# Optimization experiments

Measured on AMD Instinct MI355X. Metric: run time of the kernel, lower is better.

Reference implementation:

```python
import jax, jax.numpy as jnp
from jax import lax
import numpy as np

B, N, DIM = 2, 2048, 1024
HEADS, DIM_HEAD = 16, 64
KERNELS = (0, 3, 5, 7)
GROUPS = len(KERNELS)
HPG = HEADS // GROUPS          # heads per group = 4
CG = HPG * DIM_HEAD            # channels per group for depthwise conv = 256
INNER = HEADS * DIM_HEAD       # 1024


def _alibi_slopes(n):
    # power-of-2 branch of LearnedAlibiPosBias._get_slopes (n=4 here)
    start = 2.0 ** (-(2.0 ** -(np.log2(n) - 3)))
    return np.array([start * start ** i for i in range(n)], dtype=np.float32)


def setup_inputs() -> dict:
    key = jax.random.key(0)
    ks = jax.random.split(key, 24)
    d = {}
    d['x'] = jax.random.normal(ks[0], (B, N, DIM), jnp.float32)
    d['ln_gamma'] = jnp.ones((DIM,), jnp.float32)
    d['ln_beta'] = jnp.zeros((DIM,), jnp.float32)
    d['w_qkv'] = jax.random.normal(ks[1], (3 * INNER, DIM), jnp.float32) * 0.02
    i = 2
    for p in ('q', 'k', 'v'):
        for ksz in (3, 5, 7):
            d[f'dw{p}_w{ksz}'] = jax.random.normal(ks[i], (CG, 1, ksz), jnp.float32) * 0.1; i += 1
            d[f'dw{p}_b{ksz}'] = jax.random.normal(ks[i], (CG,), jnp.float32) * 0.02; i += 1
    # learned alibi slopes, initialized to the standard ALiBi values per group
    sl = _alibi_slopes(HPG).reshape(1, HPG, 1, 1)
    d['slopes'] = jnp.asarray(np.tile(sl, (GROUPS, 1, 1, 1)))
    d['w_out'] = jax.random.normal(ks[20], (DIM, INNER), jnp.float32) * 0.02
    return d


def _dw_causal_conv(xg, w, b, ksz):
    # xg: (B, CG, N); depthwise causal conv, left pad ksz-1
    xg = jnp.pad(xg, ((0, 0), (0, 0), (ksz - 1, 0)))
    out = lax.conv_general_dilated(xg, w, (1,), 'VALID',
                                   feature_group_count=CG,
                                   dimension_numbers=('NCH', 'OIH', 'NCH'))
    return out + b[None, :, None]


def _grouped_conv(t, w3, b3, w5, b5, w7, b7):
    # t: (B, INNER, N) channels laid out head-major; group g = channels [g*CG,(g+1)*CG)
    parts = [t[:, :CG]]  # group 0: kernel_size 0 -> Identity
    for i, (w, b, ksz) in enumerate(((w3, b3, 3), (w5, b5, 5), (w7, b7, 7))):
        parts.append(_dw_causal_conv(t[:, (i + 1) * CG:(i + 2) * CG], w, b, ksz))
    out = jnp.concatenate(parts, axis=1)                      # (B, INNER, N)
    out = out.reshape(B, HEADS, DIM_HEAD, N)
    return jnp.transpose(out, (0, 1, 3, 2))                   # (B, H, N, Dh)


def _forward(x, ln_gamma, ln_beta, w_qkv,
             dwq_w3, dwq_b3, dwq_w5, dwq_b5, dwq_w7, dwq_b7,
             dwk_w3, dwk_b3, dwk_w5, dwk_b5, dwk_w7, dwk_b7,
             dwv_w3, dwv_b3, dwv_w5, dwv_b5, dwv_w7, dwv_b7,
             slopes, w_out):
    scale = DIM_HEAD ** -0.5
    mu = jnp.mean(x, axis=-1, keepdims=True)
    var = jnp.var(x, axis=-1, keepdims=True)
    h = (x - mu) * lax.rsqrt(var + 1e-5) * ln_gamma + ln_beta   # (B, N, DIM)
    qkv = jnp.einsum('bnd,ed->ben', h, w_qkv)                   # (B, 3*INNER, N)
    q, k, v = jnp.split(qkv, 3, axis=1)
    q = _grouped_conv(q, dwq_w3, dwq_b3, dwq_w5, dwq_b5, dwq_w7, dwq_b7)
    k = _grouped_conv(k, dwk_w3, dwk_b3, dwk_w5, dwk_b5, dwk_w7, dwk_b7)
    v = _grouped_conv(v, dwv_w3, dwv_b3, dwv_w5, dwv_b5, dwv_w7, dwv_b7)
    sim = jnp.einsum('bhid,bhjd->bhij', q * scale, k)           # (B, H, N, N)
    idx = jnp.arange(N)
    dist = -jnp.abs(idx[None, :] - idx[:, None]).astype(sim.dtype)  # (N, N)
    bias = slopes.reshape(HEADS, 1, 1) * dist[None]             # (H, N, N)
    sim = sim + bias[None]
    causal = idx[None, :] > idx[:, None]                        # strictly future
    sim = jnp.where(causal[None, None], -jnp.finfo(sim.dtype).max, sim)
    attn = jax.nn.softmax(sim, axis=-1)
    out = jnp.einsum('bhij,bhjd->bhid', attn, v)                # (B, H, N, Dh)
    out = jnp.transpose(out, (0, 2, 1, 3)).reshape(B, N, INNER)
    return jnp.einsum('bne,de->bnd', out, w_out)


def reference(x, ln_gamma, ln_beta, w_qkv,
              dwq_w3, dwq_b3, dwq_w5, dwq_b5, dwq_w7, dwq_b7,
              dwk_w3, dwk_b3, dwk_w5, dwk_b5, dwk_w7, dwk_b7,
              dwv_w3, dwv_b3, dwv_w5, dwv_b5, dwv_w7, dwv_b7,
              slopes, w_out):
    return _forward(x, ln_gamma, ln_beta, w_qkv,
                    dwq_w3, dwq_b3, dwq_w5, dwq_b5, dwq_w7, dwq_b7,
                    dwk_w3, dwk_b3, dwk_w5, dwk_b5, dwk_w7, dwk_b7,
                    dwv_w3, dwv_b3, dwv_w5, dwv_b5, dwv_w7, dwv_b7,
                    slopes, w_out)
```

## Files before the change

### kernel.cpp

```cpp
#include <hip/hip_runtime.h>
#include <hip/hip_bf16.h>
#include <stdint.h>

typedef __bf16 bf8 __attribute__((ext_vector_type(8)));
typedef float  f4  __attribute__((ext_vector_type(4)));

constexpr int BATCH  = 2;
constexpr int SEQ    = 2048;
constexpr int DMODEL = 1024;
constexpr int NH     = 16;
constexpr int DHEAD  = 64;
constexpr int E3     = 3072;

static __device__ __forceinline__ f4 mfma16(bf8 a, bf8 b, f4 c){
  return __builtin_amdgcn_mfma_f32_16x16x32_bf16(a, b, c, 0, 0, 0);
}
static __device__ __forceinline__ uint32_t pack2(float a, float b){
  union { __bf16 h[2]; uint32_t u; } p;
  p.h[0] = (__bf16)a; p.h[1] = (__bf16)b;
  return p.u;
}
typedef const __attribute__((address_space(1))) uint32_t g_u32;
typedef __attribute__((address_space(3))) uint32_t l_u32;
static __device__ __forceinline__ void glds16(const __bf16* g, __bf16* l){
  __builtin_amdgcn_global_load_lds((g_u32*)g, (l_u32*)l, 16, 0, 0);
}

__global__ __launch_bounds__(256) void prep_kernel(const float* __restrict__ x,
                                                   const float* __restrict__ gam,
                                                   const float* __restrict__ bet,
                                                   __bf16* __restrict__ h,
                                                   const float* __restrict__ wq,
                                                   __bf16* __restrict__ wqb){
  int bid = blockIdx.x;
  int tid = threadIdx.x;
  if(bid >= BATCH*SEQ){
    int i = ((bid - BATCH*SEQ) * 256 + tid) * 4;
    float4 v = *(const float4*)(wq + i);
    __bf16 o[4] = {(__bf16)v.x, (__bf16)v.y, (__bf16)v.z, (__bf16)v.w};
    *(uint2*)(wqb + i) = *(const uint2*)o;
    return;
  }
  int row = bid;
  const float* xr = x + (size_t)row * DMODEL;
  float4 v = *(const float4*)(xr + tid*4);
  float s = v.x + v.y + v.z + v.w;
  float ss = v.x*v.x + v.y*v.y + v.z*v.z + v.w*v.w;
#pragma unroll
  for(int m=1;m<64;m<<=1){ s += __shfl_xor(s, m); ss += __shfl_xor(ss, m); }
  __shared__ float sm[8];
  int wid = tid >> 6;
  if((tid & 63) == 0){ sm[wid] = s; sm[4+wid] = ss; }
  __syncthreads();
  s  = sm[0]+sm[1]+sm[2]+sm[3];
  ss = sm[4]+sm[5]+sm[6]+sm[7];
  float mu  = s * (1.f/DMODEL);
  float var = ss * (1.f/DMODEL) - mu*mu;
  float r = rsqrtf(var + 1e-5f);
  float4 g = *(const float4*)(gam + tid*4);
  float4 bb = *(const float4*)(bet + tid*4);
  __bf16 o[4] = { (__bf16)((v.x-mu)*r*g.x + bb.x), (__bf16)((v.y-mu)*r*g.y + bb.y),
                  (__bf16)((v.z-mu)*r*g.z + bb.z), (__bf16)((v.w-mu)*r*g.w + bb.w) };
  *(uint2*)(h + (size_t)row*DMODEL + tid*4) = *(uint2*)o;
}

template<typename CT>
__global__ __launch_bounds__(256) void gemm_nt(const __bf16* __restrict__ A,
                                               const __bf16* __restrict__ Bm,
                                               CT* __restrict__ C,
                                               int M, int Ncols, int K){
  __shared__ __align__(16) __bf16 smem[4*128*32];
  __bf16* As0 = smem;
  __bf16* Bs0 = smem + 2*128*32;
  int nwgx = gridDim.x;
  int nwg  = nwgx * gridDim.y;
  int bidl = blockIdx.y * nwgx + blockIdx.x;
  int swz  = (bidl & 7) * (nwg >> 3) + (bidl >> 3);
  int m0 = (swz / nwgx) * 128, n0 = (swz % nwgx) * 128;
  int tid = threadIdx.x;
  int lane = tid & 63, wid = tid >> 6;
  int quad = lane >> 4, l15 = lane & 15;
  int wm = (wid >> 1) * 64, wn = (wid & 1) * 64;
  f4 acc[4][4] = {};
  int r0 = wid*32 + (lane >> 2);
  int cofs = (lane & 3) * 8;
  const __bf16* ag = A  + (size_t)(m0 + r0) * K + cofs;
  const __bf16* bg = Bm + (size_t)(n0 + r0) * K + cofs;
  const int d0 = (wid*32)*32, d1 = (wid*32+16)*32;
  const size_t rowskip = (size_t)16 * K;
  glds16(ag,           As0 + d0);
  glds16(ag + rowskip, As0 + d1);
  glds16(bg,           Bs0 + d0);
  glds16(bg + rowskip, Bs0 + d1);
  __syncthreads();
  int cur = 0;
  for(int k0 = 0; k0 < K; k0 += 32){
    int k1 = k0 + 32;
    if(k1 < K){
      int nb = cur ^ 1;
      glds16(ag + k1,           As0 + nb*128*32 + d0);
      glds16(ag + rowskip + k1, As0 + nb*128*32 + d1);
      glds16(bg + k1,           Bs0 + nb*128*32 + d0);
      glds16(bg + rowskip + k1, Bs0 + nb*128*32 + d1);
    }
    const __bf16* AsC = As0 + cur*128*32;
    const __bf16* BsC = Bs0 + cur*128*32;
    bf8 af[4], bfr[4];
#pragma unroll
    for(int i=0;i<4;i++){
      af[i]  = *(const bf8*)&AsC[(wm + i*16 + l15)*32 + quad*8];
      bfr[i] = *(const bf8*)&BsC[(wn + i*16 + l15)*32 + quad*8];
    }
#pragma unroll
    for(int mi=0;mi<4;mi++)
#pragma unroll
      for(int ni=0;ni<4;ni++)
        acc[mi][ni] = mfma16(af[mi], bfr[ni], acc[mi][ni]);
    __syncthreads();
    cur ^= 1;
  }
  if constexpr (sizeof(CT) == 2){
    __bf16* scr = smem;
    uint32_t* sp = (uint32_t*)smem;
#pragma unroll
    for(int qq=0; qq<4; qq++){
      __syncthreads();
      if((wid>>1) == (qq>>1)){
        int mi0 = (qq & 1) * 2;
#pragma unroll
        for(int mm=0; mm<2; mm++){
          int mi = mi0 + mm;
#pragma unroll
          for(int ni=0; ni<4; ni++)
#pragma unroll
            for(int r=0; r<4; r++){
              int lr = (mi - mi0)*16 + quad*4 + r;
              scr[lr*136 + wn + ni*16 + l15] = (__bf16)acc[mi][ni][r];
            }
        }
      }
      __syncthreads();
#pragma unroll
      for(int it=0; it<2; it++){
        int idx = it*256 + tid;
        int row = idx >> 4;
        int ck  = idx & 15;
        uint4 v = { sp[row*68 + ck*4 + 0], sp[row*68 + ck*4 + 1],
                    sp[row*68 + ck*4 + 2], sp[row*68 + ck*4 + 3] };
        *(uint4*)(C + (size_t)(m0 + qq*32 + row)*Ncols + n0 + ck*8) = v;
      }
    }
  } else {
    float* scr = (float*)smem;
#pragma unroll
    for(int qq=0; qq<4; qq++){
      __syncthreads();
      if((wid>>1) == (qq>>1)){
        int mi0 = (qq & 1) * 2;
#pragma unroll
        for(int mm=0; mm<2; mm++){
          int mi = mi0 + mm;
#pragma unroll
          for(int ni=0; ni<4; ni++)
#pragma unroll
            for(int r=0; r<4; r++){
              int lr = (mi - mi0)*16 + quad*4 + r;
              scr[lr*136 + wn + ni*16 + l15] = acc[mi][ni][r];
            }
        }
      }
      __syncthreads();
#pragma unroll
      for(int it=0; it<4; it++){
        int idx = it*256 + tid;
        int row = idx >> 5;
        int ck  = idx & 31;
        float4 v = { scr[row*136 + ck*4 + 0], scr[row*136 + ck*4 + 1],
                     scr[row*136 + ck*4 + 2], scr[row*136 + ck*4 + 3] };
        *(float4*)(C + (size_t)(m0 + qq*32 + row)*Ncols + n0 + ck*4) = v;
      }
    }
  }
}

__global__ __launch_bounds__(256) void conv_kernel(const __bf16* __restrict__ qkv,
    __bf16* __restrict__ qo, __bf16* __restrict__ ko, __bf16* __restrict__ vt,
    const float* qw3,const float* qb3,const float* qw5,const float* qb5,const float* qw7,const float* qb7,
    const float* kw3,const float* kb3,const float* kw5,const float* kb5,const float* kw7,const float* kb7,
    const float* vw3,const float* vb3,const float* vw5,const float* vb5,const float* vw7,const float* vb7){
  __shared__ __align__(16) __bf16 tile[72*256];
  int nc = blockIdx.x;
  int ec = blockIdx.y;
  int b  = blockIdx.z;
  int tid = threadIdx.x;
  int n0 = nc * 64;
  {
    int rrow = tid >> 5;
    int ccol = (tid & 31) * 8;
    const __bf16* src = qkv + (size_t)b*SEQ*E3 + ec*256 + ccol;
#pragma unroll
    for(int p=0;p<9;p++){
      int row = p*8 + rrow;
      int n = n0 - 8 + row;
      uint4 v = {0u,0u,0u,0u};
      if(n >= 0) v = *(const uint4*)(src + (size_t)n*E3);
      *(uint4*)&tile[row*256 + ccol] = v;
    }
  }
  __syncthreads();
  int p = ec >> 2;
  int g = ec & 3;
  float w0=0.f,w1=0.f,w2=0.f,w3=0.f,w4=0.f,w5=0.f,w6=0.f,bias=0.f;
  if(g == 1){
    const float* wp = (p==0)? qw3 : (p==1)? kw3 : vw3;
    const float* bp = (p==0)? qb3 : (p==1)? kb3 : vb3;
    w0 = wp[tid*3+0]; w1 = wp[tid*3+1]; w2 = wp[tid*3+2]; bias = bp[tid];
  } else if(g == 2){
    const float* wp = (p==0)? qw5 : (p==1)? kw5 : vw5;
    const float* bp = (p==0)? qb5 : (p==1)? kb5 : vb5;
    w0 = wp[tid*5+0]; w1 = wp[tid*5+1]; w2 = wp[tid*5+2];
    w3 = wp[tid*5+3]; w4 = wp[tid*5+4]; bias = bp[tid];
  } else if(g == 3){
    const float* wp = (p==0)? qw7 : (p==1)? kw7 : vw7;
    const float* bp = (p==0)? qb7 : (p==1)? kb7 : vb7;
    w0 = wp[tid*7+0]; w1 = wp[tid*7+1]; w2 = wp[tid*7+2]; w3 = wp[tid*7+3];
    w4 = wp[tid*7+4]; w5 = wp[tid*7+5]; w6 = wp[tid*7+6]; bias = bp[tid];
  }
  float x0 = (float)tile[2*256 + tid];
  float x1 = (float)tile[3*256 + tid];
  float x2 = (float)tile[4*256 + tid];
  float x3 = (float)tile[5*256 + tid];
  float x4 = (float)tile[6*256 + tid];
  float x5 = (float)tile[7*256 + tid];
#define CONV_STEP(cur, o)                                                      \
  { if(g == 0)      o = (cur);                                                 \
    else if(g == 1) o = w0*x4 + w1*x5 + w2*(cur) + bias;                       \
    else if(g == 2) o = w0*x2 + w1*x3 + w2*x4 + w3*x5 + w4*(cur) + bias;       \
    else            o = w0*x0 + w1*x1 + w2*x2 + w3*x3 + w4*x4 + w5*x5          \
                        + w6*(cur) + bias;                                     \
    x0=x1; x1=x2; x2=x3; x3=x4; x4=x5; x5=(cur); }
  uint32_t vout[32];
#pragma unroll
  for(int blk=0; blk<8; blk++){
#pragma unroll
    for(int up=0; up<4; up++){
      float ca = (float)tile[(8 + blk*8 + up*2    )*256 + tid];
      float oa; CONV_STEP(ca, oa);
      float cb = (float)tile[(8 + blk*8 + up*2 + 1)*256 + tid];
      float ob; CONV_STEP(cb, ob);
      vout[blk*4 + up] = pack2(oa, ob);
    }
  }
#undef CONV_STEP
  __syncthreads();
  uint32_t* ot = (uint32_t*)tile;
#pragma unroll
  for(int j=0;j<32;j++) ot[tid*33 + j] = vout[j];
  __syncthreads();
  if(p == 2){
#pragma unroll
    for(int it=0; it<8; it++){
      int idx = it*256 + tid;
      int ch  = idx >> 3;
      int ncq = idx & 7;
      uint4 val = { ot[ch*33 + ncq*4 + 0], ot[ch*33 + ncq*4 + 1],
                    ot[ch*33 + ncq*4 + 2], ot[ch*33 + ncq*4 + 3] };
      int hh2 = g*4 + (ch >> 6);
      int dh2 = ch & 63;
      *(uint4*)(vt + ((size_t)((b*NH + hh2)*DHEAD + dh2))*SEQ + n0 + ncq*8) = val;
    }
  } else {
    __bf16* outp = (p==0) ? qo : ko;
#pragma unroll
    for(int it=0; it<8; it++){
      int idx = it*256 + tid;
      int lh  = idx >> 9;
      int dn  = (idx >> 3) & 63;
      int ck  = idx & 7;
      int j   = dn >> 1;
      int sh  = (dn & 1) * 16;
      uint32_t hv[8];
#pragma unroll
      for(int m=0;m<8;m++)
        hv[m] = (ot[(lh*64 + ck*8 + m)*33 + j] >> sh) & 0xffffu;
      uint4 val = { hv[0] | (hv[1]<<16), hv[2] | (hv[3]<<16),
                    hv[4] | (hv[5]<<16), hv[6] | (hv[7]<<16) };
      int hh2 = g*4 + lh;
      *(uint4*)(outp + ((size_t)(b*NH + hh2)*SEQ + n0 + dn)*DHEAD + ck*8) = val;
    }
  }
}

__global__ __launch_bounds__(256, 3) void attn_kernel(const __bf16* __restrict__ Qin,
                                                      const __bf16* __restrict__ Kin,
                                                      const __bf16* __restrict__ Vtin,
                                                      const float* __restrict__ slopes,
                                                      __bf16* __restrict__ Oout,
                                                      const float* __restrict__ wsrc,
                                                      __bf16* __restrict__ wdst){
  __shared__ __align__(16) __bf16 Ks[2][64*64];
  __shared__ __align__(16) __bf16 Vts[2][64*64];
  __shared__ __align__(16) __bf16 Ps[4][16*72];
  __shared__ float Al[4][16];
  int bid = blockIdx.x;
  int tid = threadIdx.x;
  if(bid >= 1024){
    int i = ((bid - 1024) * 256 + tid) * 4;
    float4 v = *(const float4*)(wsrc + i);
    __bf16 o[4] = {(__bf16)v.x, (__bf16)v.y, (__bf16)v.z, (__bf16)v.w};
    *(uint2*)(wdst + i) = *(const uint2*)o;
    return;
  }
  int qi = 31 - (bid >> 5);
  int by = (bid & 7) + ((bid >> 3) & 3) * 8;
  int b  = by >> 4, hh = by & 15;
  int lane = tid & 63, w = tid >> 6;
  int quad = lane >> 4, l15 = lane & 15;
  const __bf16* qb  = Qin  + (size_t)by * SEQ * DHEAD;
  const __bf16* kb  = Kin  + (size_t)by * SEQ * DHEAD;
  const __bf16* vtb = Vtin + (size_t)by * DHEAD * SEQ;
  const float L2E = 1.4426950408889634f;
  float slope = slopes[hh];
  const float c1 = 0.125f * L2E;
  float c2 = slope * L2E;
  float cjb[16];
#pragma unroll
  for(int jt=0;jt<4;jt++)
#pragma unroll
    for(int r=0;r<4;r++)
      cjb[jt*4+r] = c2 * (float)(jt*16 + quad*4 + r);

  int sxq0 = ((quad     ^ (l15 & 7)) << 3);
  int sxq1 = (((quad+4) ^ (l15 & 7)) << 3);

  int r8 = lane >> 3;
  int c8 = lane & 7;
  int sw = (c8 ^ r8) * 8;
  const __bf16* ksrc = kb  + (size_t)r8*DHEAD + sw;
  const __bf16* vsrc = vtb + (size_t)r8*SEQ  + sw;
  int g0 = w*2, g1 = w*2 + 1;
  const size_t kg0o = (size_t)g0*8*DHEAD, kg1o = (size_t)g1*8*DHEAD;
  const size_t vg0o = (size_t)g0*8*SEQ,   vg1o = (size_t)g1*8*SEQ;

  int q0 = qi * 64;
  int nst = qi + 1;
  int i0 = q0 + w*16;
  int i  = i0 + l15;
  bf8 aq0 = *(const bf8*)(qb + (size_t)i*DHEAD + quad*8);
  bf8 aq1 = *(const bf8*)(qb + (size_t)i*DHEAD + 32 + quad*8);
  f4 oacc[4] = {};
  float l_ = 0.f;
  glds16(ksrc + kg0o, &Ks[0][g0*512]);
  glds16(ksrc + kg1o, &Ks[0][g1*512]);
  glds16(vsrc + vg0o, &Vts[0][g0*512]);
  glds16(vsrc + vg1o, &Vts[0][g1*512]);
  __syncthreads();
  int cur = 0;
  for(int t=0; t<nst; t++){
    int j0 = t*64;
    bool pf = (t+1) < nst;
    if(pf){
      int nb = cur ^ 1;
      size_t off = (size_t)(t+1)*64;
      glds16(ksrc + off*DHEAD + kg0o, &Ks[nb][g0*512]);
      glds16(ksrc + off*DHEAD + kg1o, &Ks[nb][g1*512]);
      glds16(vsrc + vg0o + off,       &Vts[nb][g0*512]);
      glds16(vsrc + vg1o + off,       &Vts[nb][g1*512]);
    }
    const __bf16* KsC  = Ks[cur];
    const __bf16* VtsC = Vts[cur];
    f4 s[4] = {};
    __builtin_amdgcn_s_setprio(1);
#pragma unroll
    for(int jt=0;jt<4;jt++){
      bf8 ak0 = *(const bf8*)&KsC[(jt*16+l15)*64 + sxq0];
      bf8 ak1 = *(const bf8*)&KsC[(jt*16+l15)*64 + sxq1];
      s[jt] = mfma16(ak0, aq0, s[jt]);
      s[jt] = mfma16(ak1, aq1, s[jt]);
    }
    __builtin_amdgcn_s_setprio(0);
    bf8 bv[2][4];
#pragma unroll
    for(int jk=0;jk<2;jk++)
#pragma unroll
      for(int nd=0;nd<4;nd++)
        bv[jk][nd] = *(const bf8*)&VtsC[(nd*16+l15)*64 + (((jk*4+quad) ^ (l15&7)) << 3)];
    float sv[4][4];
    if(t < nst-1){
      float cdi = c2 * (float)(i - j0) + 8.0f;
#pragma unroll
      for(int jt=0;jt<4;jt++)
#pragma unroll
        for(int r=0;r<4;r++)
          sv[jt][r] = fmaf(s[jt][r], c1, cjb[jt*4+r] - cdi);
    } else {
#pragma unroll
      for(int jt=0;jt<4;jt++)
#pragma unroll
        for(int r=0;r<4;r++){
          int j = j0 + jt*16 + quad*4 + r;
          int d = i - j;
          float val = fmaf(s[jt][r], c1, -fmaf(c2, (float)d, 8.0f));
          sv[jt][r] = (d < 0) ? -1e30f : val;
        }
    }
    float lsum = 0.f;
#pragma unroll
    for(int jt=0;jt<4;jt++){
      float p0 = __builtin_amdgcn_exp2f(sv[jt][0]);
      float p1 = __builtin_amdgcn_exp2f(sv[jt][1]);
      float p2 = __builtin_amdgcn_exp2f(sv[jt][2]);
      float p3 = __builtin_amdgcn_exp2f(sv[jt][3]);
      lsum += (p0+p1)+(p2+p3);
      uint2 pk = { pack2(p0,p1), pack2(p2,p3) };
      *(uint2*)&Ps[w][l15*72 + jt*16 + quad*4] = pk;
    }
    lsum += __shfl_xor(lsum, 16);
    lsum += __shfl_xor(lsum, 32);
    l_ += lsum;
    __builtin_amdgcn_s_setprio(1);
#pragma unroll
    for(int jk=0;jk<2;jk++){
      bf8 ap = *(const bf8*)&Ps[w][l15*72 + jk*32 + quad*8];
#pragma unroll
      for(int nd=0;nd<4;nd++)
        oacc[nd] = mfma16(ap, bv[jk][nd], oacc[nd]);
    }
    __builtin_amdgcn_s_setprio(0);
    __syncthreads();
    cur ^= 1;
  }
  if(quad == 0) Al[w][l15] = 1.0f / l_;
  f4 linv = *(const f4*)&Al[w][quad*4];
#pragma unroll
  for(int nd=0;nd<4;nd++)
#pragma unroll
    for(int r=0;r<4;r++){
      int io = i0 + quad*4 + r;
      Oout[((size_t)(b*SEQ + io))*DMODEL + hh*64 + nd*16 + l15] =
          (__bf16)(oacc[nd][r] * linv[r]);
    }
}

extern "C" void kernel_launch(void* const* d_in, const int* in_sizes, int n_in,
                              void* d_out, int out_size, void* d_ws, size_t ws_size,
                              hipStream_t stream){
  const float* x      = (const float*)d_in[0];
  const float* gam    = (const float*)d_in[1];
  const float* bet    = (const float*)d_in[2];
  const float* w_qkv  = (const float*)d_in[3];
  const float* slopes = (const float*)d_in[22];
  const float* w_out  = (const float*)d_in[23];
  float* out = (float*)d_out;

  char* ws = (char*)d_ws;
  __bf16* h       = (__bf16*)(ws);
  __bf16* qpost   = (__bf16*)(ws);
  __bf16* qkv     = (__bf16*)(ws + ((size_t)8  << 20));
  __bf16* att     = (__bf16*)(ws + ((size_t)8  << 20));
  __bf16* wout_bf = (__bf16*)(ws + ((size_t)24 << 20));
  __bf16* wqkv_bf = (__bf16*)(ws + ((size_t)32 << 20));
  __bf16* kpost   = (__bf16*)(ws + ((size_t)32 << 20));
  __bf16* vtp     = (__bf16*)(ws + ((size_t)40 << 20));

  constexpr int NQKV = 3 * DMODEL * DMODEL;

  prep_kernel<<<BATCH*SEQ + NQKV/4/256, 256, 0, stream>>>(x, gam, bet, h, w_qkv, wqkv_bf);
  gemm_nt<__bf16><<<dim3(E3/128, (BATCH*SEQ)/128), 256, 0, stream>>>(
      h, wqkv_bf, qkv, BATCH*SEQ, E3, DMODEL);
  conv_kernel<<<dim3(32, 12, BATCH), 256, 0, stream>>>(qkv, qpost, kpost, vtp,
    (const float*)d_in[4],(const float*)d_in[5],(const float*)d_in[6],(const float*)d_in[7],
    (const float*)d_in[8],(const float*)d_in[9],
    (const float*)d_in[10],(const float*)d_in[11],(const float*)d_in[12],(const float*)d_in[13],
    (const float*)d_in[14],(const float*)d_in[15],
    (const float*)d_in[16],(const float*)d_in[17],(const float*)d_in[18],(const float*)d_in[19],
    (const float*)d_in[20],(const float*)d_in[21]);
  attn_kernel<<<dim3(2048), 256, 0, stream>>>(qpost, kpost, vtp, slopes, att,
                                              w_out, wout_bf);
  gemm_nt<float><<<dim3(DMODEL/128, (BATCH*SEQ)/128), 256, 0, stream>>>(
      att, wout_bf, out, BATCH*SEQ, DMODEL, DMODEL);
}
```

Measured before the change: 229.4 us.

## Use 256x128 tile GEMM with 512 threads for QKV projection

Adds a new GEMM kernel for the QKV projection that uses 256x128 output tiles with 8 waves, each computing a 64x64 sub-tile, and stages the bf16 output through shared memory for coalesced stores. The larger M tile raises data reuse of the B operand and halves the number of workgroups. In exchange the grid drops to 384 blocks, which can leave compute units unevenly loaded, and the epilogue adds 8 staged store passes with barriers.

After: 228.1 us. Within noise of the previous version (-0.6%).

```diff
diff --git a/kernel.cpp b/kernel.cpp
--- a/kernel.cpp
+++ b/kernel.cpp
@@ -62,6 +62,90 @@
   __bf16 o[4] = { (__bf16)((v.x-mu)*r*g.x + bb.x), (__bf16)((v.y-mu)*r*g.y + bb.y),
                   (__bf16)((v.z-mu)*r*g.z + bb.z), (__bf16)((v.w-mu)*r*g.w + bb.w) };
   *(uint2*)(h + (size_t)row*DMODEL + tid*4) = *(uint2*)o;
+}
+
+__global__ __launch_bounds__(512) void gemm_nt256(const __bf16* __restrict__ A,
+                                                  const __bf16* __restrict__ Bm,
+                                                  __bf16* __restrict__ C,
+                                                  int M, int Ncols, int K){
+  __shared__ __align__(16) __bf16 smem[2*256*32 + 2*128*32];
+  __bf16* As0 = smem;
+  __bf16* Bs0 = smem + 2*256*32;
+  int nwgx = gridDim.x;
+  int nwg  = nwgx * gridDim.y;
+  int bidl = blockIdx.y * nwgx + blockIdx.x;
+  int swz  = (bidl & 7) * (nwg >> 3) + (bidl >> 3);
+  int m0 = (swz / nwgx) * 256, n0 = (swz % nwgx) * 128;
+  int tid = threadIdx.x;
+  int lane = tid & 63, wid = tid >> 6;
+  int quad = lane >> 4, l15 = lane & 15;
+  int wm = (wid >> 1) * 64, wn = (wid & 1) * 64;
+  f4 acc[4][4] = {};
+  int ra = wid*32 + (lane >> 2);
+  int rb = wid*16 + (lane >> 2);
+  int cofs = (lane & 3) * 8;
+  const __bf16* ag = A  + (size_t)(m0 + ra) * K + cofs;
+  const __bf16* bg = Bm + (size_t)(n0 + rb) * K + cofs;
+  const int da0 = (wid*32)*32, da1 = (wid*32+16)*32, db = (wid*16)*32;
+  const size_t rowskip = (size_t)16 * K;
+  glds16(ag,           As0 + da0);
+  glds16(ag + rowskip, As0 + da1);
+  glds16(bg,           Bs0 + db);
+  __syncthreads();
+  int cur = 0;
+  for(int k0 = 0; k0 < K; k0 += 32){
+    int k1 = k0 + 32;
+    if(k1 < K){
+      int nb = cur ^ 1;
+      glds16(ag + k1,           As0 + nb*256*32 + da0);
+      glds16(ag + rowskip + k1, As0 + nb*256*32 + da1);
+      glds16(bg + k1,           Bs0 + nb*128*32 + db);
+    }
+    const __bf16* AsC = As0 + cur*256*32;
+    const __bf16* BsC = Bs0 + cur*128*32;
+    bf8 af[4], bfr[4];
+#pragma unroll
+    for(int i=0;i<4;i++){
+      af[i]  = *(const bf8*)&AsC[(wm + i*16 + l15)*32 + quad*8];
+      bfr[i] = *(const bf8*)&BsC[(wn + i*16 + l15)*32 + quad*8];
+    }
+#pragma unroll
+    for(int mi=0;mi<4;mi++)
+#pragma unroll
+      for(int ni=0;ni<4;ni++)
+        acc[mi][ni] = mfma16(af[mi], bfr[ni], acc[mi][ni]);
+    __syncthreads();
+    cur ^= 1;
+  }
+  __bf16* scr = smem;
+  uint32_t* sp = (uint32_t*)smem;
+#pragma unroll
+  for(int qq=0; qq<8; qq++){
+    __syncthreads();
+    if((wid>>1) == (qq>>1)){
+      int mi0 = (qq & 1) * 2;
+#pragma unroll
+      for(int mm=0; mm<2; mm++){
+        int mi = mi0 + mm;
+#pragma unroll
+        for(int ni=0; ni<4; ni++)
+#pragma unroll
+          for(int r=0; r<4; r++){
+            int lr = (mi - mi0)*16 + quad*4 + r;
+            scr[lr*136 + wn + ni*16 + l15] = (__bf16)acc[mi][ni][r];
+          }
+      }
+    }
+    __syncthreads();
+    {
+      int idx = tid;
+      int row = idx >> 4;
+      int ck  = idx & 15;
+      uint4 v = { sp[row*68 + ck*4 + 0], sp[row*68 + ck*4 + 1],
+                  sp[row*68 + ck*4 + 2], sp[row*68 + ck*4 + 3] };
+      *(uint4*)(C + (size_t)(m0 + qq*32 + row)*Ncols + n0 + ck*8) = v;
+    }
+  }
 }
 
 template<typename CT>
@@ -466,7 +550,7 @@
   constexpr int NQKV = 3 * DMODEL * DMODEL;
 
   prep_kernel<<<BATCH*SEQ + NQKV/4/256, 256, 0, stream>>>(x, gam, bet, h, w_qkv, wqkv_bf);
-  gemm_nt<__bf16><<<dim3(E3/128, (BATCH*SEQ)/128), 256, 0, stream>>>(
+  gemm_nt256<<<dim3(E3/128, (BATCH*SEQ)/256), 512, 0, stream>>>(
       h, wqkv_bf, qkv, BATCH*SEQ, E3, DMODEL);
   conv_kernel<<<dim3(32, 12, BATCH), 256, 0, stream>>>(qkv, qpost, kpost, vtp,
     (const float*)d_in[4],(const float*)d_in[5],(const float*)d_in[6],(const float*)d_in[7],
```
